# Optimization experiments

Hardware: AMD Instinct MI355X
Metric: run time of the kernel (lower is better)

Reference implementation:

```python
import jax, jax.numpy as jnp
import numpy as np

B_BOUND = 3.0
K = 10
SCALE_DIM = 8
TOTAL_DIM = 16
HID = 50
N = 262144
TD = TOTAL_DIM - SCALE_DIM  # transform_dim


def setup_inputs() -> dict:
    key = jax.random.key(0)
    ks = jax.random.split(key, 7)
    s = 0.1  # small init so softmax/softplus params stay well-conditioned
    return {
        "x": jax.random.normal(ks[0], (N, TOTAL_DIM), dtype=jnp.float32),
        "w0": s * jax.random.normal(ks[1], (SCALE_DIM, HID), dtype=jnp.float32),
        "b0": jnp.zeros((HID,), jnp.float32),
        "w1": s * jax.random.normal(ks[2], (HID, HID), dtype=jnp.float32),
        "b1": jnp.zeros((HID,), jnp.float32),
        "ww": s * jax.random.normal(ks[3], (HID, TD * K), dtype=jnp.float32),
        "bw": jnp.zeros((TD * K,), jnp.float32),
        "wh": s * jax.random.normal(ks[4], (HID, TD * K), dtype=jnp.float32),
        "bh": jnp.zeros((TD * K,), jnp.float32),
        "wd": s * jax.random.normal(ks[5], (HID, TD * (K - 1)), dtype=jnp.float32),
        "bd": jnp.zeros((TD * (K - 1),), jnp.float32),
    }


def _spline_forward(x, w0, b0, w1, b1, ww, bw, wh, bh, wd, bd):
    B = B_BOUND
    zd = x[:, :SCALE_DIM]          # conditioner input [N, d]
    u = x[:, SCALE_DIM:]           # values to transform [N, D]
    n, D = u.shape

    h = jnp.tanh(zd @ w0 + b0)
    h = jnp.tanh(h @ w1 + b1)

    theta_w = jax.nn.softmax((2.0 * B * (h @ ww + bw)).reshape(n, D, K), axis=-1)
    theta_h = jax.nn.softmax((2.0 * B * (h @ wh + bh)).reshape(n, D, K), axis=-1)
    theta_d = jax.nn.softplus((h @ wd + bd).reshape(n, D, K - 1))

    # Bin edges in [-B, B] via cumsum of normalized widths/heights
    xe = jnp.concatenate(
        [jnp.full((n, D, 1), -B, u.dtype), -B + 2.0 * B * jnp.cumsum(theta_w, axis=-1)], axis=-1)  # [n,D,K+1]
    ye = jnp.concatenate(
        [jnp.full((n, D, 1), -B, u.dtype), -B + 2.0 * B * jnp.cumsum(theta_h, axis=-1)], axis=-1)
    # Knot derivatives: boundary derivatives fixed to 1 (linear tails)
    ones = jnp.ones((n, D, 1), u.dtype)
    d = jnp.concatenate([ones, theta_d, ones], axis=-1)  # [n,D,K+1]

    widths = xe[..., 1:] - xe[..., :-1]
    heights = ye[..., 1:] - ye[..., :-1]

    inside = (u > -B) & (u < B)
    uc = jnp.clip(u, -B, B)
    # per-element bin search
    idx = jnp.clip(jnp.sum((uc[..., None] >= xe[..., :-1]).astype(jnp.int32), axis=-1) - 1, 0, K - 1)
    idx = idx[..., None]
    take = lambda a: jnp.take_along_axis(a, idx, axis=-1)[..., 0]

    xk, yk = take(xe[..., :-1]), take(ye[..., :-1])
    wk, hk = take(widths), take(heights)
    dk, dk1 = take(d[..., :-1]), take(d[..., 1:])

    sk = hk / wk
    xi = (uc - xk) / wk
    om = 1.0 - xi
    denom = sk + (dk1 + dk - 2.0 * sk) * xi * om
    y = yk + hk * (sk * xi * xi + dk * xi * om) / denom
    logdet = 2.0 * jnp.log(sk) + jnp.log(dk1 * xi * xi + 2.0 * sk * xi * om + dk * om * om) - 2.0 * jnp.log(denom)

    zD = jnp.where(inside, y, u)
    ld = jnp.where(inside, logdet, 0.0)
    return jnp.concatenate([zd, zD], axis=1), jnp.sum(ld)


def reference(x, w0, b0, w1, b1, ww, bw, wh, bh, wd, bd):
    return _spline_forward(x, w0, b0, w1, b1, ww, bw, wh, bh, wd, bd)
```

## Files before the change

### kernel.cpp

```cpp
#include <hip/hip_runtime.h>

#define NROWS 262144
#define KK 10
#define BB 3.0f
#define SROW 136
#define HS 80
#define SEGF16 (16 * SROW)
#define SENT 0.54132485f

typedef _Float16 v8h __attribute__((ext_vector_type(8)));
typedef _Float16 v4h __attribute__((ext_vector_type(4)));
typedef float v4f __attribute__((ext_vector_type(4)));

#define W0_OFF 0
#define W1_OFF 256
#define WC_OFF 768
#define FRAG_TOTAL 2816
#define SLOTS_OFF (FRAG_TOTAL * 4)

#if __has_builtin(__builtin_amdgcn_exp2f)
__device__ __forceinline__ float ex2(float x) { return __builtin_amdgcn_exp2f(x); }
#else
__device__ __forceinline__ float ex2(float x) { return __expf(0.6931471805599453f * x); }
#endif
#if __has_builtin(__builtin_amdgcn_rcpf)
__device__ __forceinline__ float frcp(float x) { return __builtin_amdgcn_rcpf(x); }
#else
__device__ __forceinline__ float frcp(float x) { return __fdividef(1.0f, x); }
#endif

#define LOG2E 1.4426950408889634f
#define C6 (6.0f * LOG2E)
#define CT (2.0f * LOG2E)

__device__ __forceinline__ float fast_tanh(float a) {
    const float e = ex2(CT * a);
    return fmaf(-2.0f, frcp(e + 1.0f), 1.0f);
}

__device__ __forceinline__ float softplus1(float v) {
    return fmaxf(v, 0.0f) + __logf(1.0f + ex2(-LOG2E * fabsf(v)));
}

__device__ __forceinline__ void spline_task(
    const _Float16* __restrict__ sg, int base, float ud, int g, int d,
    float* __restrict__ out, float& ldacc)
{
    float vals[32];
    #pragma unroll
    for (int blk = 0; blk < 4; ++blk) {
        const v8h p = *(const v8h*)&sg[base + blk * 8];
        #pragma unroll
        for (int j = 0; j < 8; ++j) vals[8 * blk + j] = (float)p[j];
    }

    float mw = vals[0];
    #pragma unroll
    for (int i = 1; i < KK; ++i) mw = fmaxf(mw, vals[i]);
    const float mw8 = mw * C6;
    float sw = 0.0f;
    #pragma unroll
    for (int i = 0; i < KK; ++i) { vals[i] = ex2(fmaf(vals[i], C6, -mw8)); sw += vals[i]; }
    const float invw = frcp(sw);

    float mh = vals[10];
    #pragma unroll
    for (int i = 1; i < KK; ++i) mh = fmaxf(mh, vals[10 + i]);
    const float mh8 = mh * C6;
    float sh = 0.0f;
    #pragma unroll
    for (int i = 0; i < KK; ++i) { vals[10 + i] = ex2(fmaf(vals[10 + i], C6, -mh8)); sh += vals[10 + i]; }
    const float invh = frcp(sh);

    const float uc = fminf(fmaxf(ud, -BB), BB);
    const bool inside = (ud > -BB) && (ud < BB);

    float cw = 0.0f, ch = 0.0f;
    float xprev = -BB, yprev = -BB, rprev = SENT;
    float xk = -BB, yk = -BB, wk = 1.0f, hk2 = 1.0f, rdk = SENT, rdk1 = SENT;
    #pragma unroll
    for (int i = 0; i < KK; ++i) {
        cw += vals[i] * invw;
        ch += vals[10 + i] * invh;
        const float xnext = fmaf(6.0f, cw, -BB);
        const float ynext = fmaf(6.0f, ch, -BB);
        const float rnext = (i == KK - 1) ? SENT : vals[20 + i];
        const bool c = (i == 0) || (uc >= xprev);
        if (c) { xk = xprev; yk = yprev; wk = xnext - xprev; hk2 = ynext - yprev; rdk = rprev; rdk1 = rnext; }
        xprev = xnext; yprev = ynext; rprev = rnext;
    }
    const float dk = softplus1(rdk);
    const float dk1 = softplus1(rdk1);

    const float rwk = frcp(wk);
    const float sk = hk2 * rwk;
    const float xi = (uc - xk) * rwk;
    const float om = 1.0f - xi;
    const float denom = sk + (dk1 + dk - 2.0f * sk) * xi * om;
    const float rden = frcp(denom);
    const float ynum = sk * xi * xi + dk * xi * om;
    const float yv = yk + hk2 * ynum * rden;
    const float larg = dk1 * xi * xi + 2.0f * sk * xi * om + dk * om * om;
    const float ldet = __logf(sk * sk * larg * rden * rden);

    out[g * 16 + 8 + d] = inside ? yv : ud;
    ldacc += inside ? ldet : 0.0f;
}

__global__ __launch_bounds__(256) void nsf_prep(
    const float* __restrict__ w0, const float* __restrict__ b0,
    const float* __restrict__ w1, const float* __restrict__ b1,
    const float* __restrict__ ww, const float* __restrict__ bw,
    const float* __restrict__ wh, const float* __restrict__ bh,
    const float* __restrict__ wd, const float* __restrict__ bd,
    v8h* __restrict__ wsv, float* __restrict__ wsf)
{
    const int t = blockIdx.x * 256 + threadIdx.x;
    if (t < 64) wsf[SLOTS_OFF + t] = 0.0f;
    if (t >= FRAG_TOTAL) return;

    v8h v;
    #pragma unroll
    for (int j = 0; j < 8; ++j) v[j] = (_Float16)0.0f;

    if (t < W1_OFF) {
        const int tile = t >> 6, lane = t & 63, q = lane >> 4, n = tile * 16 + (lane & 15);
        if (n < 50) {
            #pragma unroll
            for (int j = 0; j < 8; ++j) {
                const int k = q * 8 + j;
                if (k < 8)       v[j] = (_Float16)w0[k * 50 + n];
                else if (k == 8) v[j] = (_Float16)b0[n];
            }
        }
    } else if (t < WC_OFF) {
        int p = t - W1_OFF;
        const int step = p >> 8; p &= 255;
        const int tile = p >> 6, lane = p & 63, q = lane >> 4, n = tile * 16 + (lane & 15);
        if (n < 50) {
            #pragma unroll
            for (int j = 0; j < 8; ++j) {
                const int k = step * 32 + q * 8 + j;
                if (k < 50)       v[j] = (_Float16)w1[k * 50 + n];
                else if (k == 50) v[j] = (_Float16)b1[n];
            }
        }
    } else {
        int p = t - WC_OFF;
        const int step = p >> 10; p &= 1023;
        const int tile = p >> 6, lane = p & 63, q = lane >> 4;
        const int cp = tile * 16 + (lane & 15);
        const int d = cp >> 5, jj = cp & 31;
        #pragma unroll
        for (int j = 0; j < 8; ++j) {
            const int k = step * 32 + q * 8 + j;
            float val = 0.0f;
            if (k < 50) {
                if (jj < 10)      val = ww[k * 80 + d * 10 + jj];
                else if (jj < 20) val = wh[k * 80 + d * 10 + (jj - 10)];
                else if (jj < 29) val = wd[k * 72 + d * 9 + (jj - 20)];
            } else if (k == 50) {
                if (jj < 10)      val = bw[d * 10 + jj];
                else if (jj < 20) val = bh[d * 10 + (jj - 10)];
                else if (jj < 29) val = bd[d * 9 + (jj - 20)];
            }
            v[j] = (_Float16)val;
        }
    }
    wsv[t] = v;
}

__global__ __launch_bounds__(64, 2) void nsf_main_v5(
    const float* __restrict__ x,
    const v8h* __restrict__ wsv,
    float* __restrict__ out, float* __restrict__ slots)
{
    __shared__ __align__(16) _Float16 smem[2 * SEGF16];
    const int lane = threadIdx.x & 63;
    const int q = lane >> 4, l15 = lane & 15;
    _Float16* segA = &smem[0];
    _Float16* segB = &smem[SEGF16];
    const int R0 = blockIdx.x * 32;

    const float4* xv = (const float4*)x;
    float4* ov = (float4*)out;

    const float uA0 = x[(R0 + l15) * 16 + 8 + q];
    const float uA1 = x[(R0 + l15) * 16 + 12 + q];
    const float uB0 = x[(R0 + 16 + l15) * 16 + 8 + q];
    const float uB1 = x[(R0 + 16 + l15) * 16 + 12 + q];

    {
        const int gg = R0 + (lane >> 1);
        const int part = lane & 1;
        ov[gg * 4 + part] = xv[gg * 4 + part];
    }

    v8h aA, aB;
    #pragma unroll
    for (int j = 0; j < 8; ++j) { aA[j] = (_Float16)0.0f; aB[j] = (_Float16)0.0f; }
    if (lane < 16) {
        const float4 f0 = xv[(R0 + lane) * 4 + 0];
        const float4 f1 = xv[(R0 + lane) * 4 + 1];
        aA[0] = (_Float16)f0.x; aA[1] = (_Float16)f0.y; aA[2] = (_Float16)f0.z; aA[3] = (_Float16)f0.w;
        aA[4] = (_Float16)f1.x; aA[5] = (_Float16)f1.y; aA[6] = (_Float16)f1.z; aA[7] = (_Float16)f1.w;
        const float4 g0 = xv[(R0 + 16 + lane) * 4 + 0];
        const float4 g1 = xv[(R0 + 16 + lane) * 4 + 1];
        aB[0] = (_Float16)g0.x; aB[1] = (_Float16)g0.y; aB[2] = (_Float16)g0.z; aB[3] = (_Float16)g0.w;
        aB[4] = (_Float16)g1.x; aB[5] = (_Float16)g1.y; aB[6] = (_Float16)g1.z; aB[7] = (_Float16)g1.w;
    }
    if (q == 1) { aA[0] = (_Float16)1.0f; aB[0] = (_Float16)1.0f; }

    #pragma unroll
    for (int t = 0; t < 4; ++t) {
        const v8h b = wsv[W0_OFF + t * 64 + lane];
        v4f cA = __builtin_amdgcn_mfma_f32_16x16x32_f16(b, aA, (v4f)(0.0f), 0, 0, 0);
        v4f cB = __builtin_amdgcn_mfma_f32_16x16x32_f16(b, aB, (v4f)(0.0f), 0, 0, 0);
        v4h pA, pB;
        #pragma unroll
        for (int rg = 0; rg < 4; ++rg) {
            pA[rg] = (_Float16)fast_tanh(cA[rg]);
            pB[rg] = (_Float16)fast_tanh(cB[rg]);
        }
        const int o = l15 * HS + t * 16 + q * 4;
        *(v4h*)&segA[o] = pA;
        *(v4h*)&segB[o] = pB;
    }

    v8h A0A, A1A, A0B, A1B;
    A0A = *(const v8h*)&segA[l15 * HS + q * 8];
    A1A = *(const v8h*)&segA[l15 * HS + 32 + q * 8];
    A0B = *(const v8h*)&segB[l15 * HS + q * 8];
    A1B = *(const v8h*)&segB[l15 * HS + 32 + q * 8];
    if (q == 2) { A1A[2] = (_Float16)1.0f; A1B[2] = (_Float16)1.0f; }
    #pragma unroll
    for (int t = 0; t < 4; ++t) {
        const v8h bf0 = wsv[W1_OFF + t * 64 + lane];
        const v8h bf1 = wsv[W1_OFF + 256 + t * 64 + lane];
        v4f cA = __builtin_amdgcn_mfma_f32_16x16x32_f16(bf0, A0A, (v4f)(0.0f), 0, 0, 0);
        cA = __builtin_amdgcn_mfma_f32_16x16x32_f16(bf1, A1A, cA, 0, 0, 0);
        v4f cB = __builtin_amdgcn_mfma_f32_16x16x32_f16(bf0, A0B, (v4f)(0.0f), 0, 0, 0);
        cB = __builtin_amdgcn_mfma_f32_16x16x32_f16(bf1, A1B, cB, 0, 0, 0);
        v4h pA, pB;
        #pragma unroll
        for (int rg = 0; rg < 4; ++rg) {
            pA[rg] = (_Float16)fast_tanh(cA[rg]);
            pB[rg] = (_Float16)fast_tanh(cB[rg]);
        }
        const int o = l15 * HS + t * 16 + q * 4;
        *(v4h*)&segA[o] = pA;
        *(v4h*)&segB[o] = pB;
    }

    A0A = *(const v8h*)&segA[l15 * HS + q * 8];
    A1A = *(const v8h*)&segA[l15 * HS + 32 + q * 8];
    A0B = *(const v8h*)&segB[l15 * HS + q * 8];
    A1B = *(const v8h*)&segB[l15 * HS + 32 + q * 8];
    if (q == 2) { A1A[2] = (_Float16)1.0f; A1B[2] = (_Float16)1.0f; }

    float ldacc = 0.0f;

    #pragma unroll 2
    for (int t = 0; t < 8; ++t) {
        const v8h bf0 = wsv[WC_OFF + t * 64 + lane];
        const v8h bf1 = wsv[WC_OFF + 1024 + t * 64 + lane];
        v4f cA = __builtin_amdgcn_mfma_f32_16x16x32_f16(bf0, A0A, (v4f)(0.0f), 0, 0, 0);
        cA = __builtin_amdgcn_mfma_f32_16x16x32_f16(bf1, A1A, cA, 0, 0, 0);
        v4f cB = __builtin_amdgcn_mfma_f32_16x16x32_f16(bf0, A0B, (v4f)(0.0f), 0, 0, 0);
        cB = __builtin_amdgcn_mfma_f32_16x16x32_f16(bf1, A1B, cB, 0, 0, 0);
        v4h pA, pB;
        #pragma unroll
        for (int rg = 0; rg < 4; ++rg) { pA[rg] = (_Float16)cA[rg]; pB[rg] = (_Float16)cB[rg]; }
        const int o = l15 * SROW + t * 16 + q * 4;
        *(v4h*)&segA[o] = pA;
        *(v4h*)&segB[o] = pB;
    }

    spline_task(segA, l15 * SROW + q * 32, uA0, R0 + l15, q, out, ldacc);
    spline_task(segB, l15 * SROW + q * 32, uB0, R0 + 16 + l15, q, out, ldacc);

    #pragma unroll 2
    for (int t = 8; t < 16; ++t) {
        const v8h bf0 = wsv[WC_OFF + t * 64 + lane];
        const v8h bf1 = wsv[WC_OFF + 1024 + t * 64 + lane];
        v4f cA = __builtin_amdgcn_mfma_f32_16x16x32_f16(bf0, A0A, (v4f)(0.0f), 0, 0, 0);
        cA = __builtin_amdgcn_mfma_f32_16x16x32_f16(bf1, A1A, cA, 0, 0, 0);
        v4f cB = __builtin_amdgcn_mfma_f32_16x16x32_f16(bf0, A0B, (v4f)(0.0f), 0, 0, 0);
        cB = __builtin_amdgcn_mfma_f32_16x16x32_f16(bf1, A1B, cB, 0, 0, 0);
        v4h pA, pB;
        #pragma unroll
        for (int rg = 0; rg < 4; ++rg) { pA[rg] = (_Float16)cA[rg]; pB[rg] = (_Float16)cB[rg]; }
        const int o = l15 * SROW + (t - 8) * 16 + q * 4;
        *(v4h*)&segA[o] = pA;
        *(v4h*)&segB[o] = pB;
    }

    spline_task(segA, l15 * SROW + q * 32, uA1, R0 + l15, q + 4, out, ldacc);
    spline_task(segB, l15 * SROW + q * 32, uB1, R0 + 16 + l15, q + 4, out, ldacc);

    #pragma unroll
    for (int off = 32; off > 0; off >>= 1) ldacc += __shfl_down(ldacc, off);
    if (lane == 0) atomicAdd(&slots[blockIdx.x & 63], ldacc);
}

__global__ void nsf_finish(const float* __restrict__ slots, float* __restrict__ ldp) {
    float v = slots[threadIdx.x];
    #pragma unroll
    for (int off = 32; off > 0; off >>= 1) v += __shfl_down(v, off);
    if (threadIdx.x == 0) *ldp = v;
}

extern "C" void kernel_launch(void* const* d_in, const int* in_sizes, int n_in,
                              void* d_out, int out_size, void* d_ws, size_t ws_size,
                              hipStream_t stream) {
    const float* x  = (const float*)d_in[0];
    const float* w0 = (const float*)d_in[1];
    const float* b0 = (const float*)d_in[2];
    const float* w1 = (const float*)d_in[3];
    const float* b1 = (const float*)d_in[4];
    const float* ww = (const float*)d_in[5];
    const float* bw = (const float*)d_in[6];
    const float* wh = (const float*)d_in[7];
    const float* bh = (const float*)d_in[8];
    const float* wd = (const float*)d_in[9];
    const float* bd = (const float*)d_in[10];

    float* out = (float*)d_out;
    float* ldp = out + (size_t)NROWS * 16;
    v8h* wsv = (v8h*)d_ws;
    float* wsf = (float*)d_ws;
    float* slots = wsf + SLOTS_OFF;

    hipLaunchKernelGGL(nsf_prep, dim3((FRAG_TOTAL + 255) / 256), dim3(256), 0, stream,
                       w0, b0, w1, b1, ww, bw, wh, bh, wd, bd, wsv, wsf);
    hipLaunchKernelGGL(nsf_main_v5, dim3(NROWS / 32), dim3(64), 0, stream,
                       x, wsv, out, slots);
    hipLaunchKernelGGL(nsf_finish, dim3(1), dim3(64), 0, stream, slots, ldp);
}
```

Measured before the change: 155.7 us.

## Swizzle LDS staging layout, pack two waves per block, fold final reduction into main kernel

Rotates the per-row chunk position in shared-memory staging buffers by a lane-dependent offset so the MFMA output stores and fragment reloads spread across LDS banks instead of conflicting. Blocks now hold two waves (128 threads) with their own segments, halving the grid size. The separate finish kernel is removed: each wave bumps a completion counter and the last wave sums the slots and writes the logdet, saving a launch at the cost of an extra atomic per wave. The counter and slots must be zeroed before each call, and it is unclear whether the prep kernel does that.

```diff
diff --git a/kernel.cpp b/kernel.cpp
--- a/kernel.cpp
+++ b/kernel.cpp
@@ -7,6 +7,7 @@
 #define HS 80
 #define SEGF16 (16 * SROW)
 #define SENT 0.54132485f
+#define W_TOTAL (NROWS / 32)
 
 typedef _Float16 v8h __attribute__((ext_vector_type(8)));
 typedef _Float16 v4h __attribute__((ext_vector_type(4)));
@@ -43,13 +44,13 @@
 }
 
 __device__ __forceinline__ void spline_task(
-    const _Float16* __restrict__ sg, int base, float ud, int g, int d,
+    const _Float16* __restrict__ rowp, int cb, int rot, float ud, int g, int d,
     float* __restrict__ out, float& ldacc)
 {
     float vals[32];
     #pragma unroll
     for (int blk = 0; blk < 4; ++blk) {
-        const v8h p = *(const v8h*)&sg[base + blk * 8];
+        const v8h p = *(const v8h*)&rowp[((cb + blk + rot) & 15) * 8];
         #pragma unroll
         for (int j = 0; j < 8; ++j) vals[8 * blk + j] = (float)p[j];
     }
@@ -170,17 +171,20 @@
     wsv[t] = v;
 }
 
-__global__ __launch_bounds__(64, 2) void nsf_main_v5(
+__global__ __launch_bounds__(128) void nsf_main_v6(
     const float* __restrict__ x,
     const v8h* __restrict__ wsv,
     float* __restrict__ out, float* __restrict__ slots)
 {
-    __shared__ __align__(16) _Float16 smem[2 * SEGF16];
+    __shared__ __align__(16) _Float16 smem[4 * SEGF16];
+    const int w = threadIdx.x >> 6;
     const int lane = threadIdx.x & 63;
     const int q = lane >> 4, l15 = lane & 15;
-    _Float16* segA = &smem[0];
-    _Float16* segB = &smem[SEGF16];
-    const int R0 = blockIdx.x * 32;
+    const int rot = l15 + (l15 >> 3);
+    _Float16* segA = &smem[(2 * w) * SEGF16];
+    _Float16* segB = &smem[(2 * w + 1) * SEGF16];
+    const int waveId = blockIdx.x * 2 + w;
+    const int R0 = waveId * 32;
 
     const float4* xv = (const float4*)x;
     float4* ov = (float4*)out;
@@ -222,16 +226,21 @@
             pA[rg] = (_Float16)fast_tanh(cA[rg]);
             pB[rg] = (_Float16)fast_tanh(cB[rg]);
         }
-        const int o = l15 * HS + t * 16 + q * 4;
+        const int pc = ((2 * t + (q >> 1)) + rot) & 7;
+        const int o = l15 * HS + pc * 8 + (q & 1) * 4;
         *(v4h*)&segA[o] = pA;
         *(v4h*)&segB[o] = pB;
     }
 
     v8h A0A, A1A, A0B, A1B;
-    A0A = *(const v8h*)&segA[l15 * HS + q * 8];
-    A1A = *(const v8h*)&segA[l15 * HS + 32 + q * 8];
-    A0B = *(const v8h*)&segB[l15 * HS + q * 8];
-    A1B = *(const v8h*)&segB[l15 * HS + 32 + q * 8];
+    {
+        const int p0 = ((q + rot) & 7) * 8;
+        const int p1 = ((q + 4 + rot) & 7) * 8;
+        A0A = *(const v8h*)&segA[l15 * HS + p0];
+        A1A = *(const v8h*)&segA[l15 * HS + p1];
+        A0B = *(const v8h*)&segB[l15 * HS + p0];
+        A1B = *(const v8h*)&segB[l15 * HS + p1];
+    }
     if (q == 2) { A1A[2] = (_Float16)1.0f; A1B[2] = (_Float16)1.0f; }
     #pragma unroll
     for (int t = 0; t < 4; ++t) {
@@ -247,15 +256,20 @@
             pA[rg] = (_Float16)fast_tanh(cA[rg]);
             pB[rg] = (_Float16)fast_tanh(cB[rg]);
         }
-        const int o = l15 * HS + t * 16 + q * 4;
+        const int pc = ((2 * t + (q >> 1)) + rot) & 7;
+        const int o = l15 * HS + pc * 8 + (q & 1) * 4;
         *(v4h*)&segA[o] = pA;
         *(v4h*)&segB[o] = pB;
     }
 
-    A0A = *(const v8h*)&segA[l15 * HS + q * 8];
-    A1A = *(const v8h*)&segA[l15 * HS + 32 + q * 8];
-    A0B = *(const v8h*)&segB[l15 * HS + q * 8];
-    A1B = *(const v8h*)&segB[l15 * HS + 32 + q * 8];
+    {
+        const int p0 = ((q + rot) & 7) * 8;
+        const int p1 = ((q + 4 + rot) & 7) * 8;
+        A0A = *(const v8h*)&segA[l15 * HS + p0];
+        A1A = *(const v8h*)&segA[l15 * HS + p1];
+        A0B = *(const v8h*)&segB[l15 * HS + p0];
+        A1B = *(const v8h*)&segB[l15 * HS + p1];
+    }
     if (q == 2) { A1A[2] = (_Float16)1.0f; A1B[2] = (_Float16)1.0f; }
 
     float ldacc = 0.0f;
@@ -271,13 +285,14 @@
         v4h pA, pB;
         #pragma unroll
         for (int rg = 0; rg < 4; ++rg) { pA[rg] = (_Float16)cA[rg]; pB[rg] = (_Float16)cB[rg]; }
-        const int o = l15 * SROW + t * 16 + q * 4;
+        const int pc = ((2 * t + (q >> 1)) + rot) & 15;
+        const int o = l15 * SROW + pc * 8 + (q & 1) * 4;
         *(v4h*)&segA[o] = pA;
         *(v4h*)&segB[o] = pB;
     }
 
-    spline_task(segA, l15 * SROW + q * 32, uA0, R0 + l15, q, out, ldacc);
-    spline_task(segB, l15 * SROW + q * 32, uB0, R0 + 16 + l15, q, out, ldacc);
+    spline_task(&segA[l15 * SROW], q * 4, rot, uA0, R0 + l15, q, out, ldacc);
+    spline_task(&segB[l15 * SROW], q * 4, rot, uB0, R0 + 16 + l15, q, out, ldacc);
 
     #pragma unroll 2
     for (int t = 8; t < 16; ++t) {
@@ -290,24 +305,31 @@
         v4h pA, pB;
         #pragma unroll
         for (int rg = 0; rg < 4; ++rg) { pA[rg] = (_Float16)cA[rg]; pB[rg] = (_Float16)cB[rg]; }
-        const int o = l15 * SROW + (t - 8) * 16 + q * 4;
+        const int pc = ((2 * (t - 8) + (q >> 1)) + rot) & 15;
+        const int o = l15 * SROW + pc * 8 + (q & 1) * 4;
         *(v4h*)&segA[o] = pA;
         *(v4h*)&segB[o] = pB;
     }
 
-    spline_task(segA, l15 * SROW + q * 32, uA1, R0 + l15, q + 4, out, ldacc);
-    spline_task(segB, l15 * SROW + q * 32, uB1, R0 + 16 + l15, q + 4, out, ldacc);
+    spline_task(&segA[l15 * SROW], q * 4, rot, uA1, R0 + l15, q + 4, out, ldacc);
+    spline_task(&segB[l15 * SROW], q * 4, rot, uB1, R0 + 16 + l15, q + 4, out, ldacc);
 
     #pragma unroll
     for (int off = 32; off > 0; off >>= 1) ldacc += __shfl_down(ldacc, off);
-    if (lane == 0) atomicAdd(&slots[blockIdx.x & 63], ldacc);
-}
-
-__global__ void nsf_finish(const float* __restrict__ slots, float* __restrict__ ldp) {
-    float v = slots[threadIdx.x];
-    #pragma unroll
-    for (int off = 32; off > 0; off >>= 1) v += __shfl_down(v, off);
-    if (threadIdx.x == 0) *ldp = v;
+    int last = 0;
+    if (lane == 0) {
+        atomicAdd(&slots[waveId & 31], ldacc);
+        __threadfence();
+        const unsigned old = atomicAdd((unsigned int*)&slots[63], 1u);
+        last = (old == (unsigned)(W_TOTAL - 1)) ? 1 : 0;
+    }
+    last = __shfl(last, 0);
+    if (last) {
+        float v = (lane < 32) ? atomicAdd(&slots[lane], 0.0f) : 0.0f;
+        #pragma unroll
+        for (int off = 32; off > 0; off >>= 1) v += __shfl_down(v, off);
+        if (lane == 0) out[(size_t)NROWS * 16] = v;
+    }
 }
 
 extern "C" void kernel_launch(void* const* d_in, const int* in_sizes, int n_in,
@@ -326,14 +348,12 @@
     const float* bd = (const float*)d_in[10];
 
     float* out = (float*)d_out;
-    float* ldp = out + (size_t)NROWS * 16;
     v8h* wsv = (v8h*)d_ws;
     float* wsf = (float*)d_ws;
     float* slots = wsf + SLOTS_OFF;
 
     hipLaunchKernelGGL(nsf_prep, dim3((FRAG_TOTAL + 255) / 256), dim3(256), 0, stream,
                        w0, b0, w1, b1, ww, bw, wh, bh, wd, bd, wsv, wsf);
-    hipLaunchKernelGGL(nsf_main_v5, dim3(NROWS / 32), dim3(64), 0, stream,
+    hipLaunchKernelGGL(nsf_main_v6, dim3(NROWS / 64), dim3(128), 0, stream,
                        x, wsv, out, slots);
-    hipLaunchKernelGGL(nsf_finish, dim3(1), dim3(64), 0, stream, slots, ldp);
-}
+}
```

Result: slower. 326.0 us (+109.4%).
